# Optimization experiments

Measured on AMD Instinct MI355X. Metric: run time of the kernel, lower is better.

## Reference

```python
import jax, jax.numpy as jnp
import numpy as np

D, H, W_IMG = 3, 128, 128
ZDIM, HDIM = 64, 512
KSEG, B = 8, 256
DIN = D * H * W_IMG


def setup_inputs() -> dict:
    key = jax.random.key(0)
    ks = jax.random.split(key, 18)
    s = 0.02
    inp = {
        "x": jax.random.normal(ks[0], (B, D, H, W_IMG), jnp.float32),
        "K": KSEG,
        "eps0": jax.random.normal(ks[1], (B, ZDIM), jnp.float32),
        "eps_q": jax.random.normal(ks[2], (KSEG - 1, B, ZDIM), jnp.float32),
        "eps_p": jax.random.normal(ks[3], (KSEG - 1, B, ZDIM), jnp.float32),
        # encoder stem (flattened image -> hdim) and gaussian head (hdim -> 2*zdim)
        "W_stem": jax.random.normal(ks[4], (DIN, HDIM), jnp.float32) * s,
        "b_stem": jnp.zeros((HDIM,), jnp.float32),
        "W_g": jax.random.normal(ks[5], (HDIM, 2 * ZDIM), jnp.float32) * s,
        "b_g": jnp.zeros((2 * ZDIM,), jnp.float32),
        # posterior LSTM (input zdim+hdim, hidden 2*zdim); initial state is always
        # zero in the original code (state is never fed back), so W_hh drops out.
        "Wih_q": jax.random.normal(ks[6], (ZDIM + HDIM, 8 * ZDIM), jnp.float32) * s,
        "b_q": jnp.zeros((8 * ZDIM,), jnp.float32),
        "Wlin_q": jax.random.normal(ks[7], (2 * ZDIM, 2 * ZDIM), jnp.float32) * s,
        "blin_q": jnp.zeros((2 * ZDIM,), jnp.float32),
        # prior LSTM (input zdim, hidden 2*zdim)
        "Wih_p": jax.random.normal(ks[8], (ZDIM, 8 * ZDIM), jnp.float32) * s,
        "b_p": jnp.zeros((8 * ZDIM,), jnp.float32),
        "Wlin_p": jax.random.normal(ks[9], (2 * ZDIM, 2 * ZDIM), jnp.float32) * s,
        "blin_p": jnp.zeros((2 * ZDIM,), jnp.float32),
        # decoder: zdim -> 1*h*w
        "W_dec": jax.random.normal(ks[10], (ZDIM, H * W_IMG), jnp.float32) * s,
        "b_dec": jnp.zeros((H * W_IMG,), jnp.float32),
    }
    return inp


def _std(logvar):
    return jax.nn.softplus(logvar + 0.5) + 1e-8


def _lstm_step_zero_state(xin, Wih, b):
    # single LSTM step with zero initial (h, c); W_hh contribution vanishes.
    g = xin @ Wih + b
    i, f, gg, o = jnp.split(g, 4, axis=-1)  # torch gate order i,f,g,o
    c = jax.nn.sigmoid(i) * jnp.tanh(gg)
    return jax.nn.sigmoid(o) * jnp.tanh(c)


def _kl_normal(mq, sq, mp, sp):
    return jnp.log(sp / sq) + (sq * sq + (mq - mp) ** 2) / (2.0 * sp * sp) - 0.5


def reference(x, K, eps0, eps_q, eps_p, W_stem, b_stem, W_g, b_g,
              Wih_q, b_q, Wlin_q, blin_q, Wih_p, b_p, Wlin_p, blin_p,
              W_dec, b_dec):
    batch = x.shape[0]
    xf = x.reshape(batch, -1)
    hf = jax.nn.relu(xf @ W_stem + b_stem)              # [B, hdim]
    enc = hf @ W_g + b_g
    mu, logvar = jnp.split(enc, 2, axis=1)
    s0 = _std(logvar)
    z0 = mu + s0 * eps0
    kl0 = -jnp.log(s0) + (s0 * s0 + mu * mu) / 2.0 - 0.5  # KL(q || N(0,1))

    def step(z_prev, eps_pair):
        eq, ep = eps_pair
        hq = _lstm_step_zero_state(jnp.concatenate([hf, z_prev], axis=1), Wih_q, b_q)
        enc_q = hq @ Wlin_q + blin_q
        mq, lq = jnp.split(enc_q, 2, axis=1)
        sq = _std(lq)
        zq = mq + sq * eq
        hp = _lstm_step_zero_state(z_prev, Wih_p, b_p)
        enc_p = hp @ Wlin_p + blin_p
        mp, lp = jnp.split(enc_p, 2, axis=1)
        sp = _std(lp)
        kl = _kl_normal(mq, sq, mp, sp)
        return zq, (zq, kl)

    _, (zq_s, kl_s) = jax.lax.scan(step, z0, (eps_q, eps_p))
    zs = jnp.concatenate([z0[None], zq_s], axis=0)       # [K, B, zdim]

    dec = (zs.reshape(K * batch, ZDIM) @ W_dec + b_dec)
    dec = dec.reshape(K, batch, 1, H, W_IMG)
    ls = jax.nn.log_sigmoid(dec)
    lns = jax.nn.log_sigmoid(-dec)
    log_ss_excl = jnp.cumsum(lns, axis=0) - lns          # exclusive prefix sum
    log_ms = log_ss_excl + ls                            # [K, B, 1, H, W]

    kl_all = jnp.concatenate([kl0[..., None], jnp.moveaxis(kl_s, 0, -1)], axis=-1)
    return log_ms, kl_all
```

## Files before the change

kernel.cpp:

```cpp
#include <hip/hip_runtime.h>
#include <hip/hip_bf16.h>

#define ZD 64
#define HD 512
#define NB 256
#define KS 8
#define DIN 49152
#define DN 16384

typedef __attribute__((ext_vector_type(8))) short bf16x8;
typedef __attribute__((ext_vector_type(4))) float f32x4;

__device__ __forceinline__ ushort bfc(float x) {
  uint u = __float_as_uint(x);
  uint r = (u + 0x7FFFu + ((u >> 16) & 1u)) >> 16;
  return (ushort)r;
}
__device__ __forceinline__ uint pk2(float a, float b) {
  return (uint)bfc(a) | ((uint)bfc(b) << 16);
}
__device__ __forceinline__ uint cvtpk(float lo, float hi) {
  uint r;
  asm("v_cvt_pk_bf16_f32 %0, %1, %2" : "=v"(r) : "v"(lo), "v"(hi));
  return r;
}
__device__ __forceinline__ float lof(uint u) { return __uint_as_float(u << 16); }
__device__ __forceinline__ float hif(uint u) { return __uint_as_float(u & 0xFFFF0000u); }
__device__ __forceinline__ float softplusf_(float x) {
  return fmaxf(x, 0.f) + log1pf(expf(-fabsf(x)));
}
__device__ __forceinline__ float softplus_fast(float x) {
  float e = __expf(-fabsf(x));
  return fmaxf(x, 0.f) + __logf(1.f + e);
}
__device__ __forceinline__ float sigmoidf_(float x) {
  return 1.f / (1.f + expf(-x));
}

#define SPLITS 128
#define KCH (DIN / SPLITS)
#define BKK 32

__global__ __launch_bounds__(256, 2)
void stem_kernel(const float* __restrict__ x, const float* __restrict__ W,
                 float* __restrict__ part) {
  __shared__ float Af[256 * 32];
  __shared__ uint Bt[128 * 20];
  const int id = blockIdx.x;
  const int nt = (id >> 3) & 3;
  const int sp = (id >> 5) * 8 + (id & 7);
  const int n0 = nt * 128;
  const int tid = threadIdx.x;
  const int lane = tid & 63;
  const int wave = tid >> 6;
  const int wm = wave >> 1, wn = wave & 1;
  const int rr = lane & 15, gq = lane >> 4;

  f32x4 accr[8][4];
#pragma unroll
  for (int i = 0; i < 8; ++i)
#pragma unroll
    for (int j = 0; j < 4; ++j) accr[i][j] = (f32x4){0.f, 0.f, 0.f, 0.f};

  const int arow_b = tid >> 3;
  const int asub = tid & 7;
  const int bkq = tid >> 5, bn4 = tid & 31;
  auto* ldsA = (__attribute__((address_space(3))) uint*)Af;

#pragma unroll 1
  for (int it = 0; it < KCH / BKK; ++it) {
    const int k0 = sp * KCH + it * BKK;
    __syncthreads();
#pragma unroll
    for (int i = 0; i < 8; ++i) {
      const int row = i * 32 + arow_b;
      const int slot = asub ^ (row & 7);
      const float* g = x + (size_t)row * DIN + k0 + slot * 4;
      __builtin_amdgcn_global_load_lds(
          (const __attribute__((address_space(1))) uint*)g,
          ldsA + i * 1024 + wave * 256, 16, 0, 0);
    }
    {
      float4 vb[4];
#pragma unroll
      for (int j = 0; j < 4; ++j)
        vb[j] = *(const float4*)(W + (size_t)(k0 + bkq * 4 + j) * HD + n0 + bn4 * 4);
      const int gg = bkq >> 1, sb = bkq & 1;
#pragma unroll
      for (int c = 0; c < 4; ++c) {
        const int n = bn4 * 4 + c;
        const float* q0 = (const float*)&vb[0];
        const float* q1 = (const float*)&vb[1];
        const float* q2 = (const float*)&vb[2];
        const float* q3 = (const float*)&vb[3];
        uint lo = cvtpk(q0[c], q1[c]);
        uint hi = cvtpk(q2[c], q3[c]);
        const int rot = (gg + (n >> 2) + n) & 3;
        *(uint2*)&Bt[n * 20 + rot * 4 + sb * 2] = make_uint2(lo, hi);
      }
    }
    asm volatile("s_waitcnt vmcnt(0)" ::: "memory");
    __syncthreads();
    bf16x8 af[8], bfr[4];
#pragma unroll
    for (int mf = 0; mf < 8; ++mf) {
      const int r = wm * 128 + mf * 16 + rr;
      const int s = r & 7;
      float4 a0 = *(const float4*)&Af[r * 32 + ((gq * 2) ^ s) * 4];
      float4 a1 = *(const float4*)&Af[r * 32 + ((gq * 2 + 1) ^ s) * 4];
      uint4 au = make_uint4(cvtpk(a0.x, a0.y), cvtpk(a0.z, a0.w),
                            cvtpk(a1.x, a1.y), cvtpk(a1.z, a1.w));
      af[mf] = *(bf16x8*)&au;
    }
#pragma unroll
    for (int nf = 0; nf < 4; ++nf) {
      const int n = wn * 64 + nf * 16 + rr;
      const int rot = (gq + (n >> 2) + n) & 3;
      uint4 bu = *(const uint4*)&Bt[n * 20 + rot * 4];
      bfr[nf] = *(bf16x8*)&bu;
    }
#pragma unroll
    for (int mf = 0; mf < 8; ++mf)
#pragma unroll
      for (int nf = 0; nf < 4; ++nf)
        accr[mf][nf] = __builtin_amdgcn_mfma_f32_16x16x32_bf16(
            af[mf], bfr[nf], accr[mf][nf], 0, 0, 0);
  }

  const int ccol = lane & 15, crow = (lane >> 4) * 4;
  float* base = part + (size_t)sp * (NB * HD);
#pragma unroll
  for (int mf = 0; mf < 8; ++mf) {
#pragma unroll
    for (int nf = 0; nf < 4; ++nf) {
      const int col = n0 + wn * 64 + nf * 16 + ccol;
      const int row = wm * 128 + mf * 16 + crow;
#pragma unroll
      for (int i = 0; i < 4; ++i)
        base[(size_t)(row + i) * HD + col] = accr[mf][nf][i];
    }
  }
}

__global__ __launch_bounds__(256)
void reduce_kernel(const float* __restrict__ part, float* __restrict__ acc) {
  __shared__ float4 sh[128];
  const int f4 = blockIdx.x * 128 + (threadIdx.x & 127);
  const int half = threadIdx.x >> 7;
  const float4* p = (const float4*)part;
  float4 s = {0.f, 0.f, 0.f, 0.f};
#pragma unroll 8
  for (int sp = half * 64; sp < half * 64 + 64; ++sp) {
    float4 v = p[(size_t)sp * (NB * HD / 4) + f4];
    s.x += v.x; s.y += v.y; s.z += v.z; s.w += v.w;
  }
  if (half) sh[threadIdx.x - 128] = s;
  __syncthreads();
  if (!half) {
    float4 o = sh[threadIdx.x];
    o.x += s.x; o.y += s.y; o.z += s.z; o.w += s.w;
    ((float4*)acc)[f4] = o;
  }
}

__global__ __launch_bounds__(256)
void prep_kernel(const float* __restrict__ Wd, ushort* __restrict__ WdT,
                 const float* __restrict__ Wihq, const float* __restrict__ Wg,
                 ushort* __restrict__ WcT,
                 const float* __restrict__ Wihp,
                 const float* __restrict__ Wlinq, const float* __restrict__ Wlinp,
                 uint* __restrict__ wzq, uint* __restrict__ wzp,
                 uint* __restrict__ wlq, uint* __restrict__ wlp) {
  __shared__ float T[64][68];
  const int bx = blockIdx.x;
  const int t = threadIdx.x;
  if (bx < 64) {
    const int c = bx * 256 + t;
    uint packed[32];
#pragma unroll
    for (int k = 0; k < 32; ++k) {
      float a = Wd[(size_t)(2 * k) * DN + c];
      float b = Wd[(size_t)(2 * k + 1) * DN + c];
      packed[k] = pk2(a, b);
    }
    uint4* dst = (uint4*)&WdT[(size_t)c * 64];
#pragma unroll
    for (int i = 0; i < 8; ++i)
      dst[i] = make_uint4(packed[4 * i], packed[4 * i + 1], packed[4 * i + 2],
                          packed[4 * i + 3]);
  } else if (bx < 144) {
    const int bx2 = bx - 64;
    const int cx = bx2 % 10, ky = bx2 / 10;
    const int ct = cx * 64, kt = ky * 64;
    {
      const int rl = t >> 2, cq = (t & 3) * 16;
      const float* src = (cx < 8) ? &Wihq[(size_t)(kt + rl) * 512 + ct + cq]
                                  : &Wg[(size_t)(kt + rl) * 128 + (ct - 512) + cq];
#pragma unroll
      for (int i = 0; i < 4; ++i) {
        float4 v = *(const float4*)(src + 4 * i);
        T[rl][cq + 4 * i + 0] = v.x;
        T[rl][cq + 4 * i + 1] = v.y;
        T[rl][cq + 4 * i + 2] = v.z;
        T[rl][cq + 4 * i + 3] = v.w;
      }
    }
    __syncthreads();
    {
      const int cl = t >> 2, kq = (t & 3) * 16;
      uint* dst = (uint*)WcT;
#pragma unroll
      for (int i = 0; i < 8; ++i) {
        uint u = pk2(T[kq + 2 * i][cl], T[kq + 2 * i + 1][cl]);
        dst[(((size_t)(ct + cl)) * 512 + kt + kq + 2 * i) >> 1] = u;
      }
    }
  } else {
    const int tp = (bx - 144) * 256 + t;
#pragma unroll
    for (int r2 = 0; r2 < 4; ++r2) {
      const int i = tp * 4 + r2;
      const int zp = i >> 9, col = i & 511;
      wzq[i] = pk2(Wihq[(size_t)(HD + 2 * zp) * HD + col],
                   Wihq[(size_t)(HD + 2 * zp + 1) * HD + col]);
      wzp[i] = pk2(Wihp[(size_t)(2 * zp) * HD + col],
                   Wihp[(size_t)(2 * zp + 1) * HD + col]);
      if (i < 8192) {
        const int kp2 = i >> 7, jj = i & 127;
        wlq[i] = pk2(Wlinq[(2 * kp2) * 128 + jj], Wlinq[(2 * kp2 + 1) * 128 + jj]);
        wlp[i] = pk2(Wlinp[(2 * kp2) * 128 + jj], Wlinp[(2 * kp2 + 1) * 128 + jj]);
      }
    }
  }
}

__global__ __launch_bounds__(256)
void gemmA_kernel(const float* __restrict__ acc, const float* __restrict__ bstem,
                  const ushort* __restrict__ WcT, const float* __restrict__ bq,
                  const float* __restrict__ bg, float* __restrict__ hfqg,
                  float* __restrict__ enc0g) {
  const int tid = threadIdx.x;
  const int lane = tid & 63;
  const int wave = tid >> 6;
  const int rr = lane & 15, gq = lane >> 4;
  const int mtile = blockIdx.y * 16;
  const int ncol = blockIdx.x * 64 + wave * 16;
  const int row = mtile + rr;

  f32x4 a4 = (f32x4){0.f, 0.f, 0.f, 0.f};
#pragma unroll
  for (int ks2 = 0; ks2 < 16; ++ks2) {
    const int k0 = ks2 * 32 + gq * 8;
    float4 x0 = *(const float4*)&acc[(size_t)row * HD + k0];
    float4 x1 = *(const float4*)&acc[(size_t)row * HD + k0 + 4];
    float4 b0 = *(const float4*)&bstem[k0];
    float4 b1 = *(const float4*)&bstem[k0 + 4];
    bf16x8 af;
    af[0] = (short)bfc(fmaxf(x0.x + b0.x, 0.f));
    af[1] = (short)bfc(fmaxf(x0.y + b0.y, 0.f));
    af[2] = (short)bfc(fmaxf(x0.z + b0.z, 0.f));
    af[3] = (short)bfc(fmaxf(x0.w + b0.w, 0.f));
    af[4] = (short)bfc(fmaxf(x1.x + b1.x, 0.f));
    af[5] = (short)bfc(fmaxf(x1.y + b1.y, 0.f));
    af[6] = (short)bfc(fmaxf(x1.z + b1.z, 0.f));
    af[7] = (short)bfc(fmaxf(x1.w + b1.w, 0.f));
    bf16x8 bf = *(const bf16x8*)&WcT[(size_t)(ncol + rr) * 512 + k0];
    a4 = __builtin_amdgcn_mfma_f32_16x16x32_bf16(af, bf, a4, 0, 0, 0);
  }
  const int col = ncol + rr;
  if (col < 512) {
    const float bb = bq[col];
#pragma unroll
    for (int i = 0; i < 4; ++i)
      hfqg[(size_t)(mtile + 4 * gq + i) * HD + col] = a4[i] + bb;
  } else {
    const float bb = bg[col - 512];
#pragma unroll
    for (int i = 0; i < 4; ++i)
      enc0g[(size_t)(mtile + 4 * gq + i) * 128 + (col - 512)] = a4[i] + bb;
  }
}

__global__ __launch_bounds__(512, 2)
void scan_kernel(const float* __restrict__ hfqg, const float* __restrict__ enc0g,
                 const uint* __restrict__ wzqg, const uint* __restrict__ wzpg,
                 const uint* __restrict__ wlqg, const uint* __restrict__ wlpg,
                 const float* __restrict__ blinq, const float* __restrict__ blinp,
                 const float* __restrict__ bp,
                 const float* __restrict__ eps0, const float* __restrict__ epsq,
                 ushort* __restrict__ zsb, float* __restrict__ out_kl) {
  const int b = blockIdx.x, tid = threadIdx.x;
  __shared__ uint WlL[2][64 * 128];
  __shared__ float g[512], gp[512];
  __shared__ float hq[128], hp[128];
  __shared__ float psum[512];
  __shared__ float zsh[64];
  __shared__ float epsL[448];

  uint wq[32], wp[32];
#pragma unroll
  for (int zp = 0; zp < 32; ++zp) {
    wq[zp] = wzqg[zp * 512 + tid];
    wp[zp] = wzpg[zp * 512 + tid];
  }
#pragma unroll
  for (int i = 0; i < 16; ++i) {
    const int idx = i * 512 + tid;
    WlL[0][idx] = wlqg[idx];
    WlL[1][idx] = wlpg[idx];
  }
  if (tid < 448) epsL[tid] = epsq[(size_t)((tid >> 6) * NB + b) * ZD + (tid & 63)];
  const float hfq_reg = hfqg[(size_t)b * HD + tid];
  const float bp_reg = bp[tid];
  if (tid < 64) {
    float mu = enc0g[b * 128 + tid], lv = enc0g[b * 128 + 64 + tid];
    float s0 = softplusf_(lv + 0.5f) + 1e-8f;
    float z0 = mu + s0 * eps0[b * ZD + tid];
    zsh[tid] = z0;
    zsb[(b * KS) * ZD + tid] = bfc(z0);
    out_kl[(b * ZD + tid) * KS] = -logf(s0) + (s0 * s0 + mu * mu) * 0.5f - 0.5f;
  }
  __syncthreads();

  for (int t = 0; t < KS - 1; ++t) {
    float aq = hfq_reg, ap = bp_reg;
#pragma unroll
    for (int zp = 0; zp < 32; ++zp) {
      float z0v = zsh[2 * zp], z1v = zsh[2 * zp + 1];
      uint uq = wq[zp], up = wp[zp];
      aq += z0v * lof(uq) + z1v * hif(uq);
      ap += z0v * lof(up) + z1v * hif(up);
    }
    g[tid] = aq;
    gp[tid] = ap;
    __syncthreads();
    if (tid < 128) {
      float cs = sigmoidf_(g[tid]) * tanhf(g[256 + tid]);
      hq[tid] = sigmoidf_(g[384 + tid]) * tanhf(cs);
    } else if (tid < 256) {
      int j = tid & 127;
      float cs = sigmoidf_(gp[j]) * tanhf(gp[256 + j]);
      hp[j] = sigmoidf_(gp[384 + j]) * tanhf(cs);
    }
    __syncthreads();
    {
      int s = tid & 255, jj = s & 127, kc = s >> 7;
      int mq_ = tid >> 8;
      const float* h = mq_ ? hp : hq;
      const uint* W = WlL[mq_];
      float a = 0.f;
#pragma unroll
      for (int kp = 0; kp < 32; ++kp) {
        uint u = W[(kc * 32 + kp) * 128 + jj];
        a += h[kc * 64 + 2 * kp] * lof(u) + h[kc * 64 + 2 * kp + 1] * hif(u);
      }
      psum[tid] = a;
    }
    __syncthreads();
    if (tid < 64) {
      float mq = psum[tid] + psum[128 + tid] + blinq[tid];
      float lq = psum[64 + tid] + psum[192 + tid] + blinq[64 + tid];
      float sq = softplusf_(lq + 0.5f) + 1e-8f;
      float zq = mq + sq * epsL[t * 64 + tid];
      float mp2 = psum[256 + tid] + psum[384 + tid] + blinp[tid];
      float lp = psum[320 + tid] + psum[448 + tid] + blinp[64 + tid];
      float sp_ = softplusf_(lp + 0.5f) + 1e-8f;
      float d = mq - mp2;
      out_kl[(b * ZD + tid) * KS + t + 1] =
          logf(sp_ / sq) + (sq * sq + d * d) / (2.f * sp_ * sp_) - 0.5f;
      zsb[(b * KS + t + 1) * ZD + tid] = bfc(zq);
      zsh[tid] = zq;
    }
    __syncthreads();
  }
}

__global__ __launch_bounds__(256)
void dec_kernel(const ushort* __restrict__ zsb, const ushort* __restrict__ WdT,
                const float* __restrict__ bd, float* __restrict__ out) {
  const int tid = threadIdx.x;
  const int lane = tid & 63;
  const int wave = tid >> 6;
  const int rr = lane & 15, gq = lane >> 4;
  const int mtile0 = blockIdx.y * 32;
  const int ncol0 = blockIdx.x * 256 + wave * 64;

  bf16x8 bfr[2][4];
#pragma unroll
  for (int ks2 = 0; ks2 < 2; ++ks2)
#pragma unroll
    for (int nf = 0; nf < 4; ++nf)
      bfr[ks2][nf] = *(const bf16x8*)&WdT[(size_t)(ncol0 + nf * 16 + rr) * 64 +
                                          ks2 * 32 + gq * 8];
  bf16x8 af[2][2];
#pragma unroll
  for (int mi = 0; mi < 2; ++mi)
#pragma unroll
    for (int ks2 = 0; ks2 < 2; ++ks2)
      af[mi][ks2] = *(const bf16x8*)&zsb[(size_t)(mtile0 + mi * 16 + rr) * 64 +
                                         ks2 * 32 + gq * 8];
  float bde[4];
#pragma unroll
  for (int nf = 0; nf < 4; ++nf) bde[nf] = bd[ncol0 + nf * 16 + rr];

  f32x4 acc[2][4];
#pragma unroll
  for (int mi = 0; mi < 2; ++mi)
#pragma unroll
    for (int nf = 0; nf < 4; ++nf) acc[mi][nf] = (f32x4){0.f, 0.f, 0.f, 0.f};

#pragma unroll
  for (int mi = 0; mi < 2; ++mi)
#pragma unroll
    for (int ks2 = 0; ks2 < 2; ++ks2)
#pragma unroll
      for (int nf = 0; nf < 4; ++nf)
        acc[mi][nf] = __builtin_amdgcn_mfma_f32_16x16x32_bf16(
            af[mi][ks2], bfr[ks2][nf], acc[mi][nf], 0, 0, 0);

  const int khi = (gq & 1) * 4;
#pragma unroll
  for (int mi = 0; mi < 2; ++mi) {
    const int bb = ((mtile0 + mi * 16) >> 3) + (gq >> 1);
#pragma unroll
    for (int nf = 0; nf < 4; ++nf) {
      const int col = ncol0 + nf * 16 + rr;
      float run = 0.f;
      float ov[4];
#pragma unroll
      for (int i = 0; i < 4; ++i) {
        float dec = acc[mi][nf][i] + bde[nf];
        float spd = softplus_fast(dec);
        ov[i] = run + (dec - spd);
        run -= spd;
      }
      float prev = __shfl_xor(run, 16, 64);
      float base = (gq & 1) ? prev : 0.f;
#pragma unroll
      for (int i = 0; i < 4; ++i)
        out[((size_t)(khi + i) * NB + bb) * DN + col] = ov[i] + base;
    }
  }
}

extern "C" void kernel_launch(void* const* d_in, const int* in_sizes, int n_in,
                              void* d_out, int out_size, void* d_ws, size_t ws_size,
                              hipStream_t stream) {
  (void)in_sizes; (void)n_in; (void)out_size; (void)ws_size;
  const float* x     = (const float*)d_in[0];
  const float* eps0  = (const float*)d_in[2];
  const float* epsq  = (const float*)d_in[3];
  const float* Wstem = (const float*)d_in[5];
  const float* bstem = (const float*)d_in[6];
  const float* Wg    = (const float*)d_in[7];
  const float* bgp   = (const float*)d_in[8];
  const float* Wihq  = (const float*)d_in[9];
  const float* bq    = (const float*)d_in[10];
  const float* Wlinq = (const float*)d_in[11];
  const float* blinq = (const float*)d_in[12];
  const float* Wihp  = (const float*)d_in[13];
  const float* bp    = (const float*)d_in[14];
  const float* Wlinp = (const float*)d_in[15];
  const float* blinp = (const float*)d_in[16];
  const float* Wd    = (const float*)d_in[17];
  const float* bd    = (const float*)d_in[18];

  float* out    = (float*)d_out;
  float* outkl  = out + (size_t)KS * NB * DN;
  float* accbuf = (float*)d_ws;
  ushort* zsb   = (ushort*)(accbuf + NB * HD);
  ushort* wdt   = zsb + (size_t)KS * NB * ZD;
  ushort* wcombT = wdt + (size_t)DN * ZD;
  float* hfqg   = (float*)(wcombT + 640 * 512);
  float* enc0g  = hfqg + NB * HD;
  uint* wzq     = (uint*)(enc0g + NB * 128);
  uint* wzp     = wzq + 32 * 512;
  uint* wlq     = wzp + 32 * 512;
  uint* wlp     = wlq + 64 * 128;
  float* part   = out;

  prep_kernel<<<160, 256, 0, stream>>>(Wd, wdt, Wihq, Wg, wcombT, Wihp,
                                       Wlinq, Wlinp, wzq, wzp, wlq, wlp);
  stem_kernel<<<4 * SPLITS, 256, 0, stream>>>(x, Wstem, part);
  reduce_kernel<<<NB * HD / 4 / 128, 256, 0, stream>>>(part, accbuf);
  gemmA_kernel<<<dim3(10, 16), 256, 0, stream>>>(accbuf, bstem, wcombT, bq, bgp,
                                                 hfqg, enc0g);
  scan_kernel<<<NB, 512, 0, stream>>>(hfqg, enc0g, wzq, wzp, wlq, wlp,
                                      blinq, blinp, bp, eps0, epsq, zsb, outkl);
  dec_kernel<<<dim3(64, 64), 256, 0, stream>>>(zsb, wdt, bd, out);
}
```

Measured before the change: 132.2 us.

## Merge weight prep into stem kernel and store split-K partials as bf16

Folds the weight-preparation kernel into the stem GEMM launch as extra blocks, removing one kernel launch and letting the prep work run alongside the stem GEMM. The per-split partial sums of the stem GEMM are now written as bf16 instead of fp32, which halves the write and read traffic of the 128-way split-K partial buffer; the reduce kernel reads them back as bf16. Rounding each of the 128 partials to bf16 before summing adds numerical error to the stem activations. The merged kernel also carries extra shared memory for the prep transpose, which may lower occupancy of the stem blocks.

```diff
diff --git a/kernel.cpp b/kernel.cpp
--- a/kernel.cpp
+++ b/kernel.cpp
@@ -26,6 +26,7 @@
 }
 __device__ __forceinline__ float lof(uint u) { return __uint_as_float(u << 16); }
 __device__ __forceinline__ float hif(uint u) { return __uint_as_float(u & 0xFFFF0000u); }
+__device__ __forceinline__ float bf2f(ushort u) { return __uint_as_float((uint)u << 16); }
 __device__ __forceinline__ float softplusf_(float x) {
   return fmaxf(x, 0.f) + log1pf(expf(-fabsf(x)));
 }
@@ -42,15 +43,87 @@
 #define BKK 32
 
 __global__ __launch_bounds__(256, 2)
-void stem_kernel(const float* __restrict__ x, const float* __restrict__ W,
-                 float* __restrict__ part) {
+void stem_prep_kernel(const float* __restrict__ x, const float* __restrict__ W,
+                      ushort* __restrict__ part,
+                      const float* __restrict__ Wd, ushort* __restrict__ WdT,
+                      const float* __restrict__ Wihq, const float* __restrict__ Wg,
+                      ushort* __restrict__ WcT, const float* __restrict__ Wihp,
+                      const float* __restrict__ Wlinq, const float* __restrict__ Wlinp,
+                      uint* __restrict__ wzq, uint* __restrict__ wzp,
+                      uint* __restrict__ wlq, uint* __restrict__ wlp) {
   __shared__ float Af[256 * 32];
   __shared__ uint Bt[128 * 20];
+  __shared__ float T[64][68];
+  const int tid = threadIdx.x;
+
+  if (blockIdx.x >= 512) {
+    const int bx = blockIdx.x - 512;
+    const int t = tid;
+    if (bx < 64) {
+      const int c = bx * 256 + t;
+      uint packed[32];
+#pragma unroll
+      for (int k = 0; k < 32; ++k) {
+        float a = Wd[(size_t)(2 * k) * DN + c];
+        float b = Wd[(size_t)(2 * k + 1) * DN + c];
+        packed[k] = pk2(a, b);
+      }
+      uint4* dst = (uint4*)&WdT[(size_t)c * 64];
+#pragma unroll
+      for (int i = 0; i < 8; ++i)
+        dst[i] = make_uint4(packed[4 * i], packed[4 * i + 1], packed[4 * i + 2],
+                            packed[4 * i + 3]);
+    } else if (bx < 144) {
+      const int bx2 = bx - 64;
+      const int cx = bx2 % 10, ky = bx2 / 10;
+      const int ct = cx * 64, kt = ky * 64;
+      {
+        const int rl = t >> 2, cq = (t & 3) * 16;
+        const float* src = (cx < 8) ? &Wihq[(size_t)(kt + rl) * 512 + ct + cq]
+                                    : &Wg[(size_t)(kt + rl) * 128 + (ct - 512) + cq];
+#pragma unroll
+        for (int i = 0; i < 4; ++i) {
+          float4 v = *(const float4*)(src + 4 * i);
+          T[rl][cq + 4 * i + 0] = v.x;
+          T[rl][cq + 4 * i + 1] = v.y;
+          T[rl][cq + 4 * i + 2] = v.z;
+          T[rl][cq + 4 * i + 3] = v.w;
+        }
+      }
+      __syncthreads();
+      {
+        const int cl = t >> 2, kq = (t & 3) * 16;
+        uint* dst = (uint*)WcT;
+#pragma unroll
+        for (int i = 0; i < 8; ++i) {
+          uint u = pk2(T[kq + 2 * i][cl], T[kq + 2 * i + 1][cl]);
+          dst[(((size_t)(ct + cl)) * 512 + kt + kq + 2 * i) >> 1] = u;
+        }
+      }
+    } else {
+      const int tp = (bx - 144) * 256 + t;
+#pragma unroll
+      for (int r2 = 0; r2 < 4; ++r2) {
+        const int i = tp * 4 + r2;
+        const int zp = i >> 9, col = i & 511;
+        wzq[i] = pk2(Wihq[(size_t)(HD + 2 * zp) * HD + col],
+                     Wihq[(size_t)(HD + 2 * zp + 1) * HD + col]);
+        wzp[i] = pk2(Wihp[(size_t)(2 * zp) * HD + col],
+                     Wihp[(size_t)(2 * zp + 1) * HD + col]);
+        if (i < 8192) {
+          const int kp2 = i >> 7, jj = i & 127;
+          wlq[i] = pk2(Wlinq[(2 * kp2) * 128 + jj], Wlinq[(2 * kp2 + 1) * 128 + jj]);
+          wlp[i] = pk2(Wlinp[(2 * kp2) * 128 + jj], Wlinp[(2 * kp2 + 1) * 128 + jj]);
+        }
+      }
+    }
+    return;
+  }
+
   const int id = blockIdx.x;
   const int nt = (id >> 3) & 3;
   const int sp = (id >> 5) * 8 + (id & 7);
   const int n0 = nt * 128;
-  const int tid = threadIdx.x;
   const int lane = tid & 63;
   const int wave = tid >> 6;
   const int wm = wave >> 1, wn = wave & 1;
@@ -128,7 +201,7 @@
   }
 
   const int ccol = lane & 15, crow = (lane >> 4) * 4;
-  float* base = part + (size_t)sp * (NB * HD);
+  ushort* base = part + (size_t)sp * (NB * HD);
 #pragma unroll
   for (int mf = 0; mf < 8; ++mf) {
 #pragma unroll
@@ -137,100 +210,29 @@
       const int row = wm * 128 + mf * 16 + crow;
 #pragma unroll
       for (int i = 0; i < 4; ++i)
-        base[(size_t)(row + i) * HD + col] = accr[mf][nf][i];
+        base[(size_t)(row + i) * HD + col] = bfc(accr[mf][nf][i]);
     }
   }
 }
 
 __global__ __launch_bounds__(256)
-void reduce_kernel(const float* __restrict__ part, float* __restrict__ acc) {
+void reduce_kernel(const ushort* __restrict__ part, float* __restrict__ acc) {
   __shared__ float4 sh[128];
-  const int f4 = blockIdx.x * 128 + (threadIdx.x & 127);
+  const int q4 = blockIdx.x * 128 + (threadIdx.x & 127);
   const int half = threadIdx.x >> 7;
-  const float4* p = (const float4*)part;
+  const ushort4* p = (const ushort4*)part;
   float4 s = {0.f, 0.f, 0.f, 0.f};
 #pragma unroll 8
   for (int sp = half * 64; sp < half * 64 + 64; ++sp) {
-    float4 v = p[(size_t)sp * (NB * HD / 4) + f4];
-    s.x += v.x; s.y += v.y; s.z += v.z; s.w += v.w;
+    ushort4 v = p[(size_t)sp * (NB * HD / 4) + q4];
+    s.x += bf2f(v.x); s.y += bf2f(v.y); s.z += bf2f(v.z); s.w += bf2f(v.w);
   }
   if (half) sh[threadIdx.x - 128] = s;
   __syncthreads();
   if (!half) {
     float4 o = sh[threadIdx.x];
     o.x += s.x; o.y += s.y; o.z += s.z; o.w += s.w;
-    ((float4*)acc)[f4] = o;
-  }
-}
-
-__global__ __launch_bounds__(256)
-void prep_kernel(const float* __restrict__ Wd, ushort* __restrict__ WdT,
-                 const float* __restrict__ Wihq, const float* __restrict__ Wg,
-                 ushort* __restrict__ WcT,
-                 const float* __restrict__ Wihp,
-                 const float* __restrict__ Wlinq, const float* __restrict__ Wlinp,
-                 uint* __restrict__ wzq, uint* __restrict__ wzp,
-                 uint* __restrict__ wlq, uint* __restrict__ wlp) {
-  __shared__ float T[64][68];
-  const int bx = blockIdx.x;
-  const int t = threadIdx.x;
-  if (bx < 64) {
-    const int c = bx * 256 + t;
-    uint packed[32];
-#pragma unroll
-    for (int k = 0; k < 32; ++k) {
-      float a = Wd[(size_t)(2 * k) * DN + c];
-      float b = Wd[(size_t)(2 * k + 1) * DN + c];
-      packed[k] = pk2(a, b);
-    }
-    uint4* dst = (uint4*)&WdT[(size_t)c * 64];
-#pragma unroll
-    for (int i = 0; i < 8; ++i)
-      dst[i] = make_uint4(packed[4 * i], packed[4 * i + 1], packed[4 * i + 2],
-                          packed[4 * i + 3]);
-  } else if (bx < 144) {
-    const int bx2 = bx - 64;
-    const int cx = bx2 % 10, ky = bx2 / 10;
-    const int ct = cx * 64, kt = ky * 64;
-    {
-      const int rl = t >> 2, cq = (t & 3) * 16;
-      const float* src = (cx < 8) ? &Wihq[(size_t)(kt + rl) * 512 + ct + cq]
-                                  : &Wg[(size_t)(kt + rl) * 128 + (ct - 512) + cq];
-#pragma unroll
-      for (int i = 0; i < 4; ++i) {
-        float4 v = *(const float4*)(src + 4 * i);
-        T[rl][cq + 4 * i + 0] = v.x;
-        T[rl][cq + 4 * i + 1] = v.y;
-        T[rl][cq + 4 * i + 2] = v.z;
-        T[rl][cq + 4 * i + 3] = v.w;
-      }
-    }
-    __syncthreads();
-    {
-      const int cl = t >> 2, kq = (t & 3) * 16;
-      uint* dst = (uint*)WcT;
-#pragma unroll
-      for (int i = 0; i < 8; ++i) {
-        uint u = pk2(T[kq + 2 * i][cl], T[kq + 2 * i + 1][cl]);
-        dst[(((size_t)(ct + cl)) * 512 + kt + kq + 2 * i) >> 1] = u;
-      }
-    }
-  } else {
-    const int tp = (bx - 144) * 256 + t;
-#pragma unroll
-    for (int r2 = 0; r2 < 4; ++r2) {
-      const int i = tp * 4 + r2;
-      const int zp = i >> 9, col = i & 511;
-      wzq[i] = pk2(Wihq[(size_t)(HD + 2 * zp) * HD + col],
-                   Wihq[(size_t)(HD + 2 * zp + 1) * HD + col]);
-      wzp[i] = pk2(Wihp[(size_t)(2 * zp) * HD + col],
-                   Wihp[(size_t)(2 * zp + 1) * HD + col]);
-      if (i < 8192) {
-        const int kp2 = i >> 7, jj = i & 127;
-        wlq[i] = pk2(Wlinq[(2 * kp2) * 128 + jj], Wlinq[(2 * kp2 + 1) * 128 + jj]);
-        wlp[i] = pk2(Wlinp[(2 * kp2) * 128 + jj], Wlinp[(2 * kp2 + 1) * 128 + jj]);
-      }
-    }
+    ((float4*)acc)[q4] = o;
   }
 }
 
@@ -477,11 +479,11 @@
   uint* wzp     = wzq + 32 * 512;
   uint* wlq     = wzp + 32 * 512;
   uint* wlp     = wlq + 64 * 128;
-  float* part   = out;
-
-  prep_kernel<<<160, 256, 0, stream>>>(Wd, wdt, Wihq, Wg, wcombT, Wihp,
-                                       Wlinq, Wlinp, wzq, wzp, wlq, wlp);
-  stem_kernel<<<4 * SPLITS, 256, 0, stream>>>(x, Wstem, part);
+  ushort* part  = (ushort*)out;
+
+  stem_prep_kernel<<<4 * SPLITS + 160, 256, 0, stream>>>(
+      x, Wstem, part, Wd, wdt, Wihq, Wg, wcombT, Wihp, Wlinq, Wlinp,
+      wzq, wzp, wlq, wlp);
   reduce_kernel<<<NB * HD / 4 / 128, 256, 0, stream>>>(part, accbuf);
   gemmA_kernel<<<dim3(10, 16), 256, 0, stream>>>(accbuf, bstem, wcombT, bq, bgp,
                                                  hfqg, enc0g);
```

New measurement: 121.5 us (median of 2 runs). 8.1% less time.
